# Optimization experiments

Hardware: AMD Instinct MI355X
Metric: run time of the kernel (lower is better)

## Reference

```python
import jax, jax.numpy as jnp
import numpy as np

N_NODES = 50000
N_EDGES = 800000
N_GRAPHS = 64
IN_DIM = 108
HID = 128
OUT_DIM = 64


def setup_inputs() -> dict:
    key = jax.random.key(0)
    ks = jax.random.split(key, 10)
    x = jax.random.normal(ks[0], (N_NODES, IN_DIM - 1), dtype=jnp.float32)
    votes = jax.random.normal(ks[1], (N_NODES, 1), dtype=jnp.float32)
    edge_index = jax.random.randint(ks[2], (2, N_EDGES), 0, N_NODES, dtype=jnp.int64)
    batch = jnp.sort(jax.random.randint(ks[3], (N_NODES,), 0, N_GRAPHS, dtype=jnp.int64))
    # SAGEConv params (PyG defaults: mean aggr; lin_l has bias, lin_r has no bias)
    s1 = 1.0 / np.sqrt(IN_DIM)
    s2 = 1.0 / np.sqrt(HID)
    W1l = jax.random.uniform(ks[4], (IN_DIM, HID), jnp.float32, -s1, s1)
    b1 = jnp.zeros((HID,), jnp.float32)
    W1r = jax.random.uniform(ks[5], (IN_DIM, HID), jnp.float32, -s1, s1)
    W2l = jax.random.uniform(ks[6], (HID, OUT_DIM), jnp.float32, -s2, s2)
    b2 = jnp.zeros((OUT_DIM,), jnp.float32)
    W2r = jax.random.uniform(ks[7], (HID, OUT_DIM), jnp.float32, -s2, s2)
    return {"x": x, "votes": votes, "edge_index": edge_index, "batch": batch,
            "W1l": W1l, "b1": b1, "W1r": W1r, "W2l": W2l, "b2": b2, "W2r": W2r}


def _sage_conv(h, src, dst, Wl, b, Wr):
    # mean-aggregate neighbor features x_j at target i, then lin_l(agg) + lin_r(x_i)
    agg = jax.ops.segment_sum(h[src], dst, num_segments=h.shape[0])  # [N, d]
    deg = jax.ops.segment_sum(jnp.ones((src.shape[0],), h.dtype), dst,
                              num_segments=h.shape[0])
    agg = agg / jnp.maximum(deg, 1.0)[:, None]
    return agg @ Wl + b + h @ Wr


def reference(x, votes, edge_index, batch, W1l, b1, W1r, W2l, b2, W2r):
    src, dst = edge_index[0], edge_index[1]
    h = jnp.concatenate([x, votes], axis=1)              # [N, 108]
    h = jax.nn.relu(_sage_conv(h, src, dst, W1l, b1, W1r))  # [N, 128]
    h = _sage_conv(h, src, dst, W2l, b2, W2r)               # [N, 64]
    return jax.ops.segment_max(h, batch, num_segments=N_GRAPHS)  # [G, 64]
```

## Files before the change

### kernel.cpp

```cpp
#include <hip/hip_runtime.h>
#include <hip/hip_bf16.h>

#define IN_F 108
#define XD   107
#define HID  128
#define OUTD 64
#define SEG_NODES 64
#define BSH 6
#define BNODES 64
#define MAXBK 1024
#define EPB 4096
#define BP1_N (8 * 7 * 64 * 8)
#define BP2_N (8 * 4 * 64 * 8)

typedef unsigned short ushort_t;
typedef unsigned int uint_t;
typedef __attribute__((ext_vector_type(8))) short bf16x8;
typedef __attribute__((ext_vector_type(4))) float f32x4;

__device__ inline void atomicMaxF(float* addr, float val) {
    if (val >= 0.f) atomicMax((int*)addr, __float_as_int(val));
    else            atomicMin((unsigned int*)addr, __float_as_uint(val));
}

__device__ inline ushort_t f2bf(float f) {
    uint_t b = __float_as_uint(f);
    return (ushort_t)((b + 0x7fffu + ((b >> 16) & 1u)) >> 16);
}

__global__ void init_out_kernel(float* out, int n) {
    int i = blockIdx.x * 256 + threadIdx.x;
    if (i < n) out[i] = -__builtin_inff();
}

__global__ __launch_bounds__(256) void bhist_kernel(const int* __restrict__ dst,
                                                    int* __restrict__ bcnt, int E, int nbk) {
    __shared__ int lh[MAXBK];
    for (int i = threadIdx.x; i < nbk; i += 256) lh[i] = 0;
    __syncthreads();
    int base = blockIdx.x * EPB;
    int end = min(base + EPB, E);
    for (int k = base + threadIdx.x; k < end; k += 256)
        atomicAdd(&lh[dst[k] >> BSH], 1);
    __syncthreads();
    for (int i = threadIdx.x; i < nbk; i += 256)
        if (lh[i] > 0) atomicAdd(&bcnt[i], lh[i]);
}

__global__ __launch_bounds__(64) void bscan_kernel(const int* __restrict__ bcnt,
                                                   int* __restrict__ bbase,
                                                   int* __restrict__ brsv,
                                                   int* __restrict__ row_start,
                                                   int nbk, int N, int E) {
    int lane = threadIdx.x;
    int carry = 0;
    for (int b = 0; b < nbk; b += 64) {
        int i = b + lane;
        int orig = (i < nbk) ? bcnt[i] : 0;
        int v = orig;
#pragma unroll
        for (int d = 1; d < 64; d <<= 1) {
            int t = __shfl_up(v, d);
            if (lane >= d) v += t;
        }
        if (i < nbk) {
            int ex = carry + v - orig;
            bbase[i] = ex;
            brsv[i] = ex;
        }
        carry += __shfl(v, 63);
    }
    if (lane == 0) {
        bbase[nbk] = E;
        row_start[N] = E;
    }
}

__global__ __launch_bounds__(256) void bscatter_kernel(const int* __restrict__ src,
                                                       const int* __restrict__ dst,
                                                       int* __restrict__ brsv,
                                                       int2* __restrict__ ebuf,
                                                       int E, int nbk) {
    __shared__ int lh[MAXBK];
    __shared__ int lofs[MAXBK];
    for (int i = threadIdx.x; i < nbk; i += 256) lh[i] = 0;
    __syncthreads();
    int base = blockIdx.x * EPB;
    int end = min(base + EPB, E);
    for (int k = base + threadIdx.x; k < end; k += 256)
        atomicAdd(&lh[dst[k] >> BSH], 1);
    __syncthreads();
    for (int i = threadIdx.x; i < nbk; i += 256)
        if (lh[i] > 0) lofs[i] = atomicAdd(&brsv[i], lh[i]);
    __syncthreads();
    for (int k = base + threadIdx.x; k < end; k += 256) {
        int d = dst[k];
        int pos = atomicAdd(&lofs[d >> BSH], 1);
        ebuf[pos] = make_int2(src[k], d);
    }
}

__global__ __launch_bounds__(256) void bbuild_kernel(const int2* __restrict__ ebuf,
                                                     const int* __restrict__ bbase,
                                                     int* __restrict__ row_start,
                                                     int* __restrict__ sorted_src,
                                                     int N) {
    __shared__ int nh[BNODES];
    __shared__ int cur[BNODES];
    int b = blockIdx.x;
    int e0 = bbase[b], e1 = bbase[b + 1];
    int nlo = b << BSH;
    int nloc = min(BNODES, N - nlo);
    if (threadIdx.x < BNODES) nh[threadIdx.x] = 0;
    __syncthreads();
    for (int k = e0 + threadIdx.x; k < e1; k += 256)
        atomicAdd(&nh[ebuf[k].y & (BNODES - 1)], 1);
    __syncthreads();
    if (threadIdx.x < 64) {
        int lane = threadIdx.x;
        int orig = nh[lane];
        int v = orig;
#pragma unroll
        for (int d = 1; d < 64; d <<= 1) {
            int t = __shfl_up(v, d);
            if (lane >= d) v += t;
        }
        int ex = e0 + v - orig;
        cur[lane] = ex;
        if (lane < nloc) row_start[nlo + lane] = ex;
    }
    __syncthreads();
    for (int k = e0 + threadIdx.x; k < e1; k += 256) {
        int2 e = ebuf[k];
        int pos = atomicAdd(&cur[e.y & (BNODES - 1)], 1);
        sorted_src[pos] = e.x;
    }
}

__global__ void convert_kernel(const float* __restrict__ x, const float* __restrict__ votes,
                               ushort_t* __restrict__ xb, int N) {
    int idx = blockIdx.x * 256 + threadIdx.x;
    if (idx >= N * IN_F) return;
    int n = idx / IN_F, f = idx - n * IN_F;
    float v = (f < XD) ? x[n * XD + f] : votes[n];
    xb[idx] = f2bf(v);
}

__global__ void convertw_kernel(const float* __restrict__ W1l, const float* __restrict__ W1r,
                                const float* __restrict__ W2l, const float* __restrict__ W2r,
                                ushort_t* __restrict__ bp1, ushort_t* __restrict__ bp2) {
    int i = blockIdx.x * 256 + threadIdx.x;
    if (i < BP1_N) {
        int j = i & 7;
        int lane = (i >> 3) & 63;
        int rest = i >> 9;
        int ks = rest % 7;
        int ct = rest / 7;
        int k = ks * 32 + (lane >> 4) * 8 + j;
        int col = ct * 16 + (lane & 15);
        float v = 0.f;
        if (k < IN_F) v = W1l[k * HID + col];
        else if (k < 2 * IN_F) v = W1r[(k - IN_F) * HID + col];
        bp1[i] = f2bf(v);
    }
    int i2 = i - BP1_N;
    if (i2 >= 0 && i2 < BP2_N) {
        int j = i2 & 7;
        int lane = (i2 >> 3) & 63;
        int ks = (i2 >> 9) & 3;
        int ct = i2 >> 11;
        int k = ks * 32 + (lane >> 4) * 8 + j;
        int col = ct * 16 + (lane & 15);
        float v = (col < OUTD) ? W2l[k * OUTD + col] : W2r[k * OUTD + (col - OUTD)];
        bp2[i2] = f2bf(v);
    }
}

__global__ __launch_bounds__(256) void gather1_kernel(
        const ushort_t* __restrict__ xb,
        const int* __restrict__ row_start, const int* __restrict__ sorted_src,
        ushort_t* __restrict__ agg1b, int N) {
    int node = (blockIdx.x * 256 + threadIdx.x) >> 6;
    int lane = threadIdx.x & 63;
    if (node >= N) return;
    int rs = row_start[node], re = row_start[node + 1];
    int h  = lane >> 5;
    int l2 = lane & 31;
    float a0 = 0.f, a1 = 0.f, a2 = 0.f, a3 = 0.f;
    for (int k0 = rs; k0 < re; k0 += 64) {
        int cnt = min(64, re - k0);
        int sl = sorted_src[k0 + min(lane, cnt - 1)];
        for (int t = 0; t < cnt; t += 2) {
            int tt = min(t + h, cnt - 1);
            int s = __shfl(sl, tt);
            if (t + h < cnt && l2 < 27) {
                uint2 w = *(const uint2*)(xb + s * IN_F + 4 * l2);
                a0 += __uint_as_float(w.x << 16);
                a1 += __uint_as_float(w.x & 0xffff0000u);
                a2 += __uint_as_float(w.y << 16);
                a3 += __uint_as_float(w.y & 0xffff0000u);
            }
        }
    }
    a0 += __shfl_xor(a0, 32);
    a1 += __shfl_xor(a1, 32);
    a2 += __shfl_xor(a2, 32);
    a3 += __shfl_xor(a3, 32);
    float inv = 1.f / fmaxf((float)(re - rs), 1.f);
    if (lane < 27) {
        ushort4 p;
        p.x = f2bf(a0 * inv);
        p.y = f2bf(a1 * inv);
        p.z = f2bf(a2 * inv);
        p.w = f2bf(a3 * inv);
        *(ushort4*)(agg1b + node * IN_F + 4 * lane) = p;
    }
}

__global__ __launch_bounds__(256) void gatheru_kernel(
        const ushort_t* __restrict__ ub,
        const int* __restrict__ row_start, const int* __restrict__ sorted_src,
        float* __restrict__ aggu, int N) {
    int node = (blockIdx.x * 256 + threadIdx.x) >> 6;
    int lane = threadIdx.x & 63;
    if (node >= N) return;
    int rs = row_start[node], re = row_start[node + 1];
    int g  = lane >> 4;
    int l4 = lane & 15;
    float a0 = 0.f, a1 = 0.f, a2 = 0.f, a3 = 0.f;
    for (int k0 = rs; k0 < re; k0 += 64) {
        int cnt = min(64, re - k0);
        int sl = sorted_src[k0 + min(lane, cnt - 1)];
        for (int t = 0; t < cnt; t += 4) {
            int tt = min(t + g, cnt - 1);
            int s = __shfl(sl, tt);
            if (t + g < cnt) {
                uint2 w = *(const uint2*)(ub + (s << 6) + 4 * l4);
                a0 += __uint_as_float(w.x << 16);
                a1 += __uint_as_float(w.x & 0xffff0000u);
                a2 += __uint_as_float(w.y << 16);
                a3 += __uint_as_float(w.y & 0xffff0000u);
            }
        }
    }
    a0 += __shfl_xor(a0, 16); a0 += __shfl_xor(a0, 32);
    a1 += __shfl_xor(a1, 16); a1 += __shfl_xor(a1, 32);
    a2 += __shfl_xor(a2, 16); a2 += __shfl_xor(a2, 32);
    a3 += __shfl_xor(a3, 16); a3 += __shfl_xor(a3, 32);
    float inv = 1.f / fmaxf((float)(re - rs), 1.f);
    if (lane < 16) {
        *(float4*)(aggu + (node << 6) + 4 * lane) =
            make_float4(a0 * inv, a1 * inv, a2 * inv, a3 * inv);
    }
}

#define T1_M 32
#define A_STRIDE_US 232
#define A_STRIDE_U  116
#define H1_STRIDE_US 136
__global__ __launch_bounds__(256) void gemm1_kernel(
        const ushort_t* __restrict__ xb, const ushort_t* __restrict__ agg1b,
        const ushort_t* __restrict__ bp1, const ushort_t* __restrict__ bp2,
        const float* __restrict__ b1,
        ushort_t* __restrict__ ub, float* __restrict__ vv, int N) {
    __shared__ uint_t smem[T1_M * A_STRIDE_U];
    int n0 = blockIdx.x * T1_M;
    for (int i = threadIdx.x; i < T1_M * 112; i += 256) {
        int m = i / 112, c = i - m * 112;
        int n = n0 + m;
        uint_t v = 0u;
        if (n < N) {
            if (c < 54)       v = ((const uint_t*)(agg1b + n * IN_F))[c];
            else if (c < 108) v = ((const uint_t*)(xb + n * IN_F))[c - 54];
        }
        smem[m * A_STRIDE_U + c] = v;
    }
    __syncthreads();

    int lane = threadIdx.x & 63;
    int wid  = threadIdx.x >> 6;
    int wrow = (wid & 1) << 4;
    int wcol = (wid >> 1) << 6;
    int arow = wrow + (lane & 15);
    int akoff = (lane >> 4) * 8;
    const ushort_t* sA = (const ushort_t*)smem;
    const bf16x8* bp1v = (const bf16x8*)bp1;

    f32x4 acc0 = {}, acc1 = {}, acc2_ = {}, acc3 = {};
    int ct0 = wcol >> 4;
#pragma unroll
    for (int ks = 0; ks < 7; ++ks) {
        bf16x8 af = *(const bf16x8*)(sA + arow * A_STRIDE_US + ks * 32 + akoff);
        bf16x8 bf0 = bp1v[((ct0 + 0) * 7 + ks) * 64 + lane];
        bf16x8 bf1 = bp1v[((ct0 + 1) * 7 + ks) * 64 + lane];
        bf16x8 bf2 = bp1v[((ct0 + 2) * 7 + ks) * 64 + lane];
        bf16x8 bf3 = bp1v[((ct0 + 3) * 7 + ks) * 64 + lane];
        acc0 = __builtin_amdgcn_mfma_f32_16x16x32_bf16(af, bf0, acc0, 0, 0, 0);
        acc1 = __builtin_amdgcn_mfma_f32_16x16x32_bf16(af, bf1, acc1, 0, 0, 0);
        acc2_ = __builtin_amdgcn_mfma_f32_16x16x32_bf16(af, bf2, acc2_, 0, 0, 0);
        acc3 = __builtin_amdgcn_mfma_f32_16x16x32_bf16(af, bf3, acc3, 0, 0, 0);
    }

    __syncthreads();
    ushort_t* sh1 = (ushort_t*)smem;
    {
        int colb = wcol + (lane & 15);
        int rowb = wrow + ((lane >> 4) << 2);
#pragma unroll
        for (int t = 0; t < 4; ++t) {
            f32x4 a = (t == 0) ? acc0 : (t == 1) ? acc1 : (t == 2) ? acc2_ : acc3;
            int col = colb + t * 16;
            float bj = b1[col];
#pragma unroll
            for (int r = 0; r < 4; ++r)
                sh1[(rowb + r) * H1_STRIDE_US + col] = f2bf(fmaxf(a[r] + bj, 0.f));
        }
    }
    __syncthreads();

    const bf16x8* bp2v = (const bf16x8*)bp2;
    f32x4 dcc0 = {}, dcc1 = {}, dcc2 = {}, dcc3 = {};
#pragma unroll
    for (int ks = 0; ks < 4; ++ks) {
        bf16x8 af = *(const bf16x8*)(sh1 + arow * H1_STRIDE_US + ks * 32 + akoff);
        bf16x8 bf0 = bp2v[((ct0 + 0) * 4 + ks) * 64 + lane];
        bf16x8 bf1 = bp2v[((ct0 + 1) * 4 + ks) * 64 + lane];
        bf16x8 bf2 = bp2v[((ct0 + 2) * 4 + ks) * 64 + lane];
        bf16x8 bf3 = bp2v[((ct0 + 3) * 4 + ks) * 64 + lane];
        dcc0 = __builtin_amdgcn_mfma_f32_16x16x32_bf16(af, bf0, dcc0, 0, 0, 0);
        dcc1 = __builtin_amdgcn_mfma_f32_16x16x32_bf16(af, bf1, dcc1, 0, 0, 0);
        dcc2 = __builtin_amdgcn_mfma_f32_16x16x32_bf16(af, bf2, dcc2, 0, 0, 0);
        dcc3 = __builtin_amdgcn_mfma_f32_16x16x32_bf16(af, bf3, dcc3, 0, 0, 0);
    }

    {
        int colb = wcol + (lane & 15);
        int rowb = wrow + ((lane >> 4) << 2);
#pragma unroll
        for (int t = 0; t < 4; ++t) {
            f32x4 a = (t == 0) ? dcc0 : (t == 1) ? dcc1 : (t == 2) ? dcc2 : dcc3;
            int col = colb + t * 16;
#pragma unroll
            for (int r = 0; r < 4; ++r) {
                int n = n0 + rowb + r;
                if (n < N) {
                    if (col < OUTD) ub[(n << 6) + col] = f2bf(a[r]);
                    else            vv[(n << 6) + (col - OUTD)] = a[r];
                }
            }
        }
    }
}

__global__ __launch_bounds__(256) void finalize_kernel(
        const float* __restrict__ aggu, const float* __restrict__ vv,
        const float* __restrict__ b2, const int* __restrict__ batch,
        float* __restrict__ out, int N) {
    int j  = threadIdx.x & 63;
    int nq = threadIdx.x >> 6;
    int n0 = blockIdx.x * SEG_NODES;
    float bj = b2[j];
    int curg = -1;
    float curm = -__builtin_inff();
    for (int m = nq; m < SEG_NODES; m += 4) {
        int n = n0 + m;
        if (n >= N) break;
        int g = batch[n];
        float v = aggu[(n << 6) + j] + vv[(n << 6) + j] + bj;
        if (g != curg) {
            if (curg >= 0) atomicMaxF(&out[(curg << 6) + j], curm);
            curg = g;
            curm = v;
        } else {
            curm = fmaxf(curm, v);
        }
    }
    if (curg >= 0) atomicMaxF(&out[(curg << 6) + j], curm);
}

static inline size_t align256(size_t v) { return (v + 255) & ~(size_t)255; }

extern "C" void kernel_launch(void* const* d_in, const int* in_sizes, int n_in,
                              void* d_out, int out_size, void* d_ws, size_t ws_size,
                              hipStream_t stream) {
    const float* x     = (const float*)d_in[0];
    const float* votes = (const float*)d_in[1];
    const int*   eidx  = (const int*)d_in[2];
    const int*   batch = (const int*)d_in[3];
    const float* W1l   = (const float*)d_in[4];
    const float* b1    = (const float*)d_in[5];
    const float* W1r   = (const float*)d_in[6];
    const float* W2l   = (const float*)d_in[7];
    const float* b2    = (const float*)d_in[8];
    const float* W2r   = (const float*)d_in[9];
    float* out = (float*)d_out;

    const int N = in_sizes[1];
    const int E = in_sizes[2] / 2;
    const int* src = eidx;
    const int* dst = eidx + E;
    const int nbk = (N + BNODES - 1) >> BSH;

    char* ws = (char*)d_ws;
    size_t off = 0;
    int* bcnt       = (int*)(ws + off); off = align256(off + (size_t)nbk * 4);
    int* bbase      = (int*)(ws + off); off = align256(off + (size_t)(nbk + 1) * 4);
    int* brsv       = (int*)(ws + off); off = align256(off + (size_t)nbk * 4);
    int* row_start  = (int*)(ws + off); off = align256(off + (size_t)(N + 1) * 4);
    int2* ebuf      = (int2*)(ws + off); off = align256(off + (size_t)E * 8);
    int* sorted_src = (int*)(ws + off); off = align256(off + (size_t)E * 4);
    ushort_t* xb    = (ushort_t*)(ws + off); off = align256(off + (size_t)N * IN_F * 2);
    ushort_t* agg1b = (ushort_t*)(ws + off); off = align256(off + (size_t)N * IN_F * 2);
    ushort_t* ub    = (ushort_t*)(ws + off); off = align256(off + (size_t)N * OUTD * 2);
    float* vv       = (float*)(ws + off); off = align256(off + (size_t)N * OUTD * 4);
    float* aggu     = (float*)(ws + off); off = align256(off + (size_t)N * OUTD * 4);
    ushort_t* bp1   = (ushort_t*)(ws + off); off = align256(off + (size_t)BP1_N * 2);
    ushort_t* bp2   = (ushort_t*)(ws + off); off = align256(off + (size_t)BP2_N * 2);

    hipMemsetAsync(bcnt, 0, (size_t)nbk * 4, stream);
    init_out_kernel<<<(out_size + 255) / 256, 256, 0, stream>>>(out, out_size);

    int nebl = (E + EPB - 1) / EPB;
    bhist_kernel<<<nebl, 256, 0, stream>>>(dst, bcnt, E, nbk);
    bscan_kernel<<<1, 64, 0, stream>>>(bcnt, bbase, brsv, row_start, nbk, N, E);
    bscatter_kernel<<<nebl, 256, 0, stream>>>(src, dst, brsv, ebuf, E, nbk);
    bbuild_kernel<<<nbk, 256, 0, stream>>>(ebuf, bbase, row_start, sorted_src, N);

    convert_kernel<<<(N * IN_F + 255) / 256, 256, 0, stream>>>(x, votes, xb, N);
    convertw_kernel<<<(BP1_N + BP2_N + 255) / 256, 256, 0, stream>>>(W1l, W1r, W2l, W2r,
                                                                     bp1, bp2);

    gather1_kernel<<<(N + 3) / 4, 256, 0, stream>>>(xb, row_start, sorted_src, agg1b, N);
    gemm1_kernel<<<(N + T1_M - 1) / T1_M, 256, 0, stream>>>(xb, agg1b, bp1, bp2,
                                                            b1, ub, vv, N);
    gatheru_kernel<<<(N + 3) / 4, 256, 0, stream>>>(ub, row_start, sorted_src, aggu, N);

    finalize_kernel<<<(N + SEG_NODES - 1) / SEG_NODES, 256, 0, stream>>>(
        aggu, vv, b2, batch, out, N);
}
```

Measured before the change: 161.7 us.

## Pack edge buffer into 32-bit words and unroll gather loops for more loads in flight

Edge records in the bucket scatter are packed into a single 32-bit word: the source index sits in the low 26 bits and the local destination index in the top 6 bits. This halves the intermediate edge-buffer traffic. Both gather kernels get an unrolled main loop that issues several independent neighbour-row loads before accumulating, to expose more memory-level parallelism. The memset is replaced by a small zeroing kernel. The packing assumes node indices fit in 26 bits, and the unrolled sums change the floating-point summation order slightly.

```diff
diff --git a/kernel.cpp b/kernel.cpp
--- a/kernel.cpp
+++ b/kernel.cpp
@@ -10,6 +10,7 @@
 #define BNODES 64
 #define MAXBK 1024
 #define EPB 4096
+#define SRCMASK 0x03FFFFFF
 #define BP1_N (8 * 7 * 64 * 8)
 #define BP2_N (8 * 4 * 64 * 8)
 
@@ -31,6 +32,11 @@
 __global__ void init_out_kernel(float* out, int n) {
     int i = blockIdx.x * 256 + threadIdx.x;
     if (i < n) out[i] = -__builtin_inff();
+}
+
+__global__ void zero_kernel(int* p, int n) {
+    int i = blockIdx.x * 256 + threadIdx.x;
+    if (i < n) p[i] = 0;
 }
 
 __global__ __launch_bounds__(256) void bhist_kernel(const int* __restrict__ dst,
@@ -79,7 +85,7 @@
 __global__ __launch_bounds__(256) void bscatter_kernel(const int* __restrict__ src,
                                                        const int* __restrict__ dst,
                                                        int* __restrict__ brsv,
-                                                       int2* __restrict__ ebuf,
+                                                       uint_t* __restrict__ ebuf,
                                                        int E, int nbk) {
     __shared__ int lh[MAXBK];
     __shared__ int lofs[MAXBK];
@@ -96,11 +102,11 @@
     for (int k = base + threadIdx.x; k < end; k += 256) {
         int d = dst[k];
         int pos = atomicAdd(&lofs[d >> BSH], 1);
-        ebuf[pos] = make_int2(src[k], d);
-    }
-}
-
-__global__ __launch_bounds__(256) void bbuild_kernel(const int2* __restrict__ ebuf,
+        ebuf[pos] = (uint_t)src[k] | ((uint_t)(d & (BNODES - 1)) << 26);
+    }
+}
+
+__global__ __launch_bounds__(256) void bbuild_kernel(const uint_t* __restrict__ ebuf,
                                                      const int* __restrict__ bbase,
                                                      int* __restrict__ row_start,
                                                      int* __restrict__ sorted_src,
@@ -114,7 +120,7 @@
     if (threadIdx.x < BNODES) nh[threadIdx.x] = 0;
     __syncthreads();
     for (int k = e0 + threadIdx.x; k < e1; k += 256)
-        atomicAdd(&nh[ebuf[k].y & (BNODES - 1)], 1);
+        atomicAdd(&nh[ebuf[k] >> 26], 1);
     __syncthreads();
     if (threadIdx.x < 64) {
         int lane = threadIdx.x;
@@ -131,9 +137,9 @@
     }
     __syncthreads();
     for (int k = e0 + threadIdx.x; k < e1; k += 256) {
-        int2 e = ebuf[k];
-        int pos = atomicAdd(&cur[e.y & (BNODES - 1)], 1);
-        sorted_src[pos] = e.x;
+        uint_t e = ebuf[k];
+        int pos = atomicAdd(&cur[e >> 26], 1);
+        sorted_src[pos] = (int)(e & SRCMASK);
     }
 }
 
@@ -190,7 +196,28 @@
     for (int k0 = rs; k0 < re; k0 += 64) {
         int cnt = min(64, re - k0);
         int sl = sorted_src[k0 + min(lane, cnt - 1)];
-        for (int t = 0; t < cnt; t += 2) {
+        int t = 0;
+        for (; t + 8 <= cnt; t += 8) {
+            int s0 = __shfl(sl, t + h);
+            int s1 = __shfl(sl, t + 2 + h);
+            int s2 = __shfl(sl, t + 4 + h);
+            int s3 = __shfl(sl, t + 6 + h);
+            if (l2 < 27) {
+                uint2 w0 = *(const uint2*)(xb + s0 * IN_F + 4 * l2);
+                uint2 w1 = *(const uint2*)(xb + s1 * IN_F + 4 * l2);
+                uint2 w2 = *(const uint2*)(xb + s2 * IN_F + 4 * l2);
+                uint2 w3 = *(const uint2*)(xb + s3 * IN_F + 4 * l2);
+                a0 += __uint_as_float(w0.x << 16) + __uint_as_float(w1.x << 16)
+                    + __uint_as_float(w2.x << 16) + __uint_as_float(w3.x << 16);
+                a1 += __uint_as_float(w0.x & 0xffff0000u) + __uint_as_float(w1.x & 0xffff0000u)
+                    + __uint_as_float(w2.x & 0xffff0000u) + __uint_as_float(w3.x & 0xffff0000u);
+                a2 += __uint_as_float(w0.y << 16) + __uint_as_float(w1.y << 16)
+                    + __uint_as_float(w2.y << 16) + __uint_as_float(w3.y << 16);
+                a3 += __uint_as_float(w0.y & 0xffff0000u) + __uint_as_float(w1.y & 0xffff0000u)
+                    + __uint_as_float(w2.y & 0xffff0000u) + __uint_as_float(w3.y & 0xffff0000u);
+            }
+        }
+        for (; t < cnt; t += 2) {
             int tt = min(t + h, cnt - 1);
             int s = __shfl(sl, tt);
             if (t + h < cnt && l2 < 27) {
@@ -231,7 +258,18 @@
     for (int k0 = rs; k0 < re; k0 += 64) {
         int cnt = min(64, re - k0);
         int sl = sorted_src[k0 + min(lane, cnt - 1)];
-        for (int t = 0; t < cnt; t += 4) {
+        int t = 0;
+        for (; t + 8 <= cnt; t += 8) {
+            int s0 = __shfl(sl, t + g);
+            int s1 = __shfl(sl, t + 4 + g);
+            uint2 w0 = *(const uint2*)(ub + (s0 << 6) + 4 * l4);
+            uint2 w1 = *(const uint2*)(ub + (s1 << 6) + 4 * l4);
+            a0 += __uint_as_float(w0.x << 16) + __uint_as_float(w1.x << 16);
+            a1 += __uint_as_float(w0.x & 0xffff0000u) + __uint_as_float(w1.x & 0xffff0000u);
+            a2 += __uint_as_float(w0.y << 16) + __uint_as_float(w1.y << 16);
+            a3 += __uint_as_float(w0.y & 0xffff0000u) + __uint_as_float(w1.y & 0xffff0000u);
+        }
+        for (; t < cnt; t += 4) {
             int tt = min(t + g, cnt - 1);
             int s = __shfl(sl, tt);
             if (t + g < cnt) {
@@ -407,7 +445,7 @@
     int* bbase      = (int*)(ws + off); off = align256(off + (size_t)(nbk + 1) * 4);
     int* brsv       = (int*)(ws + off); off = align256(off + (size_t)nbk * 4);
     int* row_start  = (int*)(ws + off); off = align256(off + (size_t)(N + 1) * 4);
-    int2* ebuf      = (int2*)(ws + off); off = align256(off + (size_t)E * 8);
+    uint_t* ebuf    = (uint_t*)(ws + off); off = align256(off + (size_t)E * 4);
     int* sorted_src = (int*)(ws + off); off = align256(off + (size_t)E * 4);
     ushort_t* xb    = (ushort_t*)(ws + off); off = align256(off + (size_t)N * IN_F * 2);
     ushort_t* agg1b = (ushort_t*)(ws + off); off = align256(off + (size_t)N * IN_F * 2);
@@ -417,7 +455,7 @@
     ushort_t* bp1   = (ushort_t*)(ws + off); off = align256(off + (size_t)BP1_N * 2);
     ushort_t* bp2   = (ushort_t*)(ws + off); off = align256(off + (size_t)BP2_N * 2);
 
-    hipMemsetAsync(bcnt, 0, (size_t)nbk * 4, stream);
+    zero_kernel<<<(nbk + 255) / 256, 256, 0, stream>>>(bcnt, nbk);
     init_out_kernel<<<(out_size + 255) / 256, 256, 0, stream>>>(out, out_size);
 
     int nebl = (E + EPB - 1) / EPB;
```

After: 148.0 us. -8.5%, faster.
